# Kernel optimization log

Measured on AMD Instinct MI355X. Metric: run time of the kernel, lower is better.

## Reference

```python
import jax, jax.numpy as jnp
import numpy as np

N, D, R, NB, E = 50000, 128, 16, 10, 1600000
DECAY_RATE = 0.1
LN_EPS = 1e-5

def setup_inputs() -> dict:
    key = jax.random.key(0)
    ks = jax.random.split(key, 12)
    x = jax.random.normal(ks[0], (N, D), dtype=jnp.float32)
    edge_index = jax.random.randint(ks[1], (2, E), 0, N, dtype=jnp.int64)
    edge_type = jax.random.randint(ks[2], (E,), 0, R, dtype=jnp.int64)
    edge_time = jax.random.uniform(ks[3], (E,), dtype=jnp.float32)
    s = 1.0 / np.sqrt(D)
    basis = jax.random.normal(ks[4], (NB, D, D), dtype=jnp.float32) * s   # RGCN basis matrices
    comp = jax.random.normal(ks[5], (R, NB), dtype=jnp.float32) * (1.0 / np.sqrt(NB))
    root = jax.random.normal(ks[6], (D, D), dtype=jnp.float32) * s        # RGCN self-loop weight
    bias = jnp.zeros((D,), dtype=jnp.float32)
    tp_w = jax.random.normal(ks[7], (D, D), dtype=jnp.float32) * s        # time_proj
    tp_b = jnp.zeros((D,), dtype=jnp.float32)
    gamma = jnp.ones((D,), dtype=jnp.float32)
    beta = jnp.zeros((D,), dtype=jnp.float32)
    return {"x": x, "edge_index": edge_index, "edge_type": edge_type, "edge_time": edge_time,
            "basis": basis, "comp": comp, "root": root, "bias": bias,
            "tp_w": tp_w, "tp_b": tp_b, "gamma": gamma, "beta": beta}

def reference(x, edge_index, edge_type, edge_time, basis, comp, root, bias, tp_w, tp_b, gamma, beta):
    n, d = x.shape
    r = comp.shape[0]
    src, dst = edge_index[0], edge_index[1]
    # ---- RGCNConv (basis decomposition, per-relation mean aggregation) ----
    W = jnp.einsum('rb,bio->rio', comp, basis)                 # [R, D, D]
    msg = x[src]                                               # [E, D] gather
    seg = dst * r + edge_type                                  # combined (node, relation) segment id
    agg = jax.ops.segment_sum(msg, seg, num_segments=n * r)    # [N*R, D]
    cnt = jax.ops.segment_sum(jnp.ones_like(seg, dtype=x.dtype), seg, num_segments=n * r)
    agg = (agg / jnp.maximum(cnt, 1.0)[:, None]).reshape(n, r, d)  # per-relation mean
    x_rgcn = jnp.einsum('nrd,rdo->no', agg, W) + x @ root + bias
    # ---- exponential time decay weights, normalized to sum 1 ----
    td = edge_time.max() - edge_time
    td = td / (td.max() + 1e-8)
    w = jnp.exp(-DECAY_RATE * td)
    w = w / (w.sum() + 1e-8)
    # ---- time-decay aggregation (sum over relations == single scatter-add) ----
    agg_t = jax.ops.segment_sum(msg * w[:, None], dst, num_segments=n)
    deg = jax.ops.segment_sum(jnp.ones_like(dst, dtype=x.dtype), dst, num_segments=n)
    x_time = agg_t / jnp.clip(deg, 1.0)[:, None]
    # ---- combine, relu, (dropout=identity in eval), layernorm ----
    xc = x_rgcn + x_time @ tp_w + tp_b
    h = jax.nn.relu(xc)
    mu = h.mean(-1, keepdims=True)
    var = ((h - mu) ** 2).mean(-1, keepdims=True)
    return (h - mu) * jax.lax.rsqrt(var + LN_EPS) * gamma + beta
```

## Files before the change

### kernel.cpp

```cpp
#include <hip/hip_runtime.h>
#include <hip/hip_bf16.h>
#include <math.h>

#define NN 50000
#define DD 128
#define RR 16
#define NBASIS 10
#define NE 1600000
#define NSEG (NN * RR)
#define NPART ((NSEG + 1023) / 1024)
#define NSLICE 12
#define KTOT (NSLICE * DD)
#define DECAY 0.1f

typedef short bf16x8 __attribute__((ext_vector_type(8)));
typedef float f32x4 __attribute__((ext_vector_type(4)));
typedef float f32x2 __attribute__((ext_vector_type(2)));

__device__ __forceinline__ ushort f2b(float f) {
    unsigned u = __float_as_uint(f);
    unsigned r = (u + 0x7FFFu + ((u >> 16) & 1u)) >> 16;
    return (ushort)r;
}
__device__ __forceinline__ unsigned cvt_pk_bf16(float lo, float hi) {
    unsigned r;
    asm("v_cvt_pk_bf16_f32 %0, %1, %2" : "=v"(r) : "v"(lo), "v"(hi));
    return r;
}


#define XB_ITEMS (NN * (DD / 4))
#define PREP_ITEMS (XB_ITEMS + DD * KTOT)
__global__ __launch_bounds__(256) void k_front(
    const int* __restrict__ edst, const int* __restrict__ etype,
    const float* __restrict__ t,
    const float* __restrict__ x, const float* __restrict__ basis,
    const float* __restrict__ root, const float* __restrict__ tp_w,
    unsigned* __restrict__ red, unsigned* __restrict__ cnt,
    unsigned* __restrict__ segrank,
    ushort* __restrict__ xb, ushort* __restrict__ Bt3)
{
    const int bid = blockIdx.x;
    const int tid = threadIdx.x;
    if (bid < 1024) {
        const int stride = 1024 * 256;
        for (int e = bid * 256 + tid; e < NE; e += stride) {
            int d  = __builtin_nontemporal_load(edst + e);
            int ty = __builtin_nontemporal_load(etype + e);
            int seg = d * RR + ty;
            unsigned sh = (unsigned)(seg & 1) << 4;
            unsigned ret = atomicAdd(&cnt[seg >> 1], 1u << sh);
            unsigned rk = (ret >> sh) & 0xFFFu;
            __builtin_nontemporal_store(((unsigned)seg << 12) | rk, segrank + e);
        }
        return;
    }
    if (bid < 2048) {
        __shared__ float smx[4], smn[4];
        float mx = 0.0f, mn = 1e30f;
        const int stride = 1024 * 256;
        for (int i = (bid - 1024) * 256 + tid; i < NE / 4; i += stride) {
            f32x4 v = __builtin_nontemporal_load(((const f32x4*)t) + i);
            mx = fmaxf(mx, fmaxf(fmaxf(v.x, v.y), fmaxf(v.z, v.w)));
            mn = fminf(mn, fminf(fminf(v.x, v.y), fminf(v.z, v.w)));
        }
        for (int o = 32; o >= 1; o >>= 1) {
            mx = fmaxf(mx, __shfl_down(mx, o, 64));
            mn = fminf(mn, __shfl_down(mn, o, 64));
        }
        if ((tid & 63) == 0) { smx[tid >> 6] = mx; smn[tid >> 6] = mn; }
        __syncthreads();
        if (tid == 0) {
            mx = fmaxf(fmaxf(smx[0], smx[1]), fmaxf(smx[2], smx[3]));
            mn = fminf(fminf(smn[0], smn[1]), fminf(smn[2], smn[3]));
            atomicMax(&red[0], __float_as_uint(mx));
            atomicMax(&red[1], ~__float_as_uint(mn));
        }
        return;
    }
    int idx = (bid - 2048) * 256 + tid;
    if (idx < XB_ITEMS) {
        f32x4 v = ((const f32x4*)x)[idx];
        uint2 o;
        o.x = cvt_pk_bf16(v.x, v.y);
        o.y = cvt_pk_bf16(v.z, v.w);
        ((uint2*)xb)[idx] = o;
        return;
    }
    int bidx = idx - XB_ITEMS;
    if (bidx >= DD * KTOT) return;
    int j = bidx / KTOT, k = bidx - j * KTOT;
    int s = k >> 7, d = k & 127;
    float v;
    if (s < NBASIS) {
        v = basis[(s * DD + d) * DD + j];
    } else if (s == NBASIS) {
        v = tp_w[d * DD + j];
    } else {
        v = root[d * DD + j];
    }
    Bt3[bidx] = f2b(v);
}

__global__ __launch_bounds__(1024) void k_scan1(const unsigned* __restrict__ cnt,
                                                unsigned* __restrict__ segptr,
                                                unsigned* __restrict__ part) {
    __shared__ unsigned sh[1024];
    int tid = threadIdx.x;
    int i = blockIdx.x * 1024 + tid;
    unsigned v = 0u;
    if (i < NSEG) v = (cnt[i >> 1] >> ((i & 1) << 4)) & 0xFFFFu;
    sh[tid] = v;
    __syncthreads();
    for (int off = 1; off < 1024; off <<= 1) {
        unsigned t = (tid >= off) ? sh[tid - off] : 0u;
        __syncthreads();
        sh[tid] += t;
        __syncthreads();
    }
    if (i < NSEG) segptr[i] = sh[tid] - v;
    if (tid == 1023) part[blockIdx.x] = sh[1023];
}

__global__ __launch_bounds__(1024) void k_scan2(unsigned* __restrict__ part) {
    __shared__ unsigned sh[1024];
    int tid = threadIdx.x;
    unsigned v = (tid < NPART) ? part[tid] : 0u;
    sh[tid] = v;
    __syncthreads();
    for (int off = 1; off < 1024; off <<= 1) {
        unsigned t = (tid >= off) ? sh[tid - off] : 0u;
        __syncthreads();
        sh[tid] += t;
        __syncthreads();
    }
    if (tid < NPART) part[tid] = sh[tid] - v;
}

__global__ __launch_bounds__(1024) void k_scan3(unsigned* __restrict__ segptr,
                                                const unsigned* __restrict__ part) {
    int i = blockIdx.x * 1024 + threadIdx.x;
    if (i < NSEG) segptr[i] += part[i >> 10];
    if (blockIdx.x == 0 && threadIdx.x == 0) segptr[NSEG] = NE;
}

__global__ __launch_bounds__(256) void k_pre2(const int* __restrict__ esrc,
                                              const float* __restrict__ etime,
                                              const unsigned* __restrict__ segrank,
                                              unsigned* __restrict__ red,
                                              const unsigned* __restrict__ segptr,
                                              unsigned* __restrict__ srcw) {
    __shared__ float ssum[4];
    const int tid = threadIdx.x;
    const float tmax = __uint_as_float(red[0]);
    const float tmin = __uint_as_float(~red[1]);
    const float rtd = -DECAY / (tmax - tmin + 1e-8f);
    float s = 0.0f;
    const int stride = gridDim.x * 256;
    for (int e = blockIdx.x * 256 + tid; e < NE; e += stride) {
        float tv    = __builtin_nontemporal_load(etime + e);
        int sv      = __builtin_nontemporal_load(esrc + e);
        unsigned sr = __builtin_nontemporal_load(segrank + e);
        float w = __expf((tmax - tv) * rtd);
        s += w;
        unsigned pos = segptr[sr >> 12] + (sr & 4095u);
        __builtin_nontemporal_store(
            (unsigned)(sv & 0xFFFF) | ((unsigned)f2b(w) << 16), srcw + pos);
    }
    for (int o = 32; o >= 1; o >>= 1) s += __shfl_down(s, o, 64);
    if ((tid & 63) == 0) ssum[tid >> 6] = s;
    __syncthreads();
    if (tid == 0)
        atomicAdd(((float*)red) + 2, ssum[0] + ssum[1] + ssum[2] + ssum[3]);
}

__global__ __launch_bounds__(256) void k_gather(
    const ushort* __restrict__ xb, const unsigned* __restrict__ srcw,
    const unsigned* __restrict__ segptr, const unsigned* __restrict__ red,
    const float* __restrict__ comp,
    ushort* __restrict__ A2)
{
    const int wave = threadIdx.x >> 6, lane = threadIdx.x & 63;
    int dst0 = blockIdx.x * 4 + wave;
    if (dst0 >= NN) return;
    const int dst = __builtin_amdgcn_readfirstlane(dst0);
    const float sumw = ((const float*)red)[2];
    const unsigned s0 = (unsigned)dst * RR;
    const unsigned start = segptr[s0];
    const unsigned endAll = segptr[s0 + RR];
    const unsigned deg = endAll - start;
    unsigned* arow = (unsigned*)(A2 + (size_t)dst * KTOT);
    const unsigned* xbu = (const unsigned*)xb;

    f32x2 cb[NBASIS];
#pragma unroll
    for (int b = 0; b < NBASIS; ++b) cb[b] = (f32x2){0.f, 0.f};
    f32x2 acc = {0.f, 0.f}, xt = {0.f, 0.f};

    int r = 0;
    unsigned scur = start;
    unsigned endr = segptr[s0 + 1];
    unsigned e = start;

#define FLUSH_REL {                                                          \
        float scl = (endr > scur) ? (1.0f / (float)(endr - scur)) : 0.0f;    \
        f32x2 t = acc * scl;                                                 \
        _Pragma("unroll")                                                    \
        for (int b = 0; b < NBASIS; ++b)                                     \
            cb[b] += t * comp[r * NBASIS + b];                               \
        acc = (f32x2){0.f, 0.f}; scur = endr; ++r;                           \
        endr = (r < RR) ? segptr[s0 + r + 1] : 0xFFFFFFFFu; }

#define ACCUM(recq, pvq) {                                                   \
        float wgt = __uint_as_float((recq) & 0xFFFF0000u);                   \
        f32x2 v;                                                             \
        v.x = __uint_as_float((pvq) << 16);                                  \
        v.y = __uint_as_float((pvq) & 0xFFFF0000u);                          \
        acc += v;                                                            \
        xt += v * wgt; }

    while (e < endAll) {
        unsigned idx = e + (unsigned)lane;
        unsigned recv = srcw[(idx < endAll) ? idx : (endAll - 1u)];
        unsigned chunk = endAll - e;
        if (chunk > 64u) chunk = 64u;
        unsigned j = 0;
        for (; j + 8u <= chunk; j += 8u) {
            unsigned rec0 = (unsigned)__builtin_amdgcn_readlane((int)recv, (int)(j + 0));
            unsigned rec1 = (unsigned)__builtin_amdgcn_readlane((int)recv, (int)(j + 1));
            unsigned rec2 = (unsigned)__builtin_amdgcn_readlane((int)recv, (int)(j + 2));
            unsigned rec3 = (unsigned)__builtin_amdgcn_readlane((int)recv, (int)(j + 3));
            unsigned rec4 = (unsigned)__builtin_amdgcn_readlane((int)recv, (int)(j + 4));
            unsigned rec5 = (unsigned)__builtin_amdgcn_readlane((int)recv, (int)(j + 5));
            unsigned rec6 = (unsigned)__builtin_amdgcn_readlane((int)recv, (int)(j + 6));
            unsigned rec7 = (unsigned)__builtin_amdgcn_readlane((int)recv, (int)(j + 7));
            unsigned pv0 = xbu[((rec0 & 0xFFFFu) << 6) + lane];
            unsigned pv1 = xbu[((rec1 & 0xFFFFu) << 6) + lane];
            unsigned pv2 = xbu[((rec2 & 0xFFFFu) << 6) + lane];
            unsigned pv3 = xbu[((rec3 & 0xFFFFu) << 6) + lane];
            unsigned pv4 = xbu[((rec4 & 0xFFFFu) << 6) + lane];
            unsigned pv5 = xbu[((rec5 & 0xFFFFu) << 6) + lane];
            unsigned pv6 = xbu[((rec6 & 0xFFFFu) << 6) + lane];
            unsigned pv7 = xbu[((rec7 & 0xFFFFu) << 6) + lane];
            while (e >= endr) FLUSH_REL; ACCUM(rec0, pv0); ++e;
            while (e >= endr) FLUSH_REL; ACCUM(rec1, pv1); ++e;
            while (e >= endr) FLUSH_REL; ACCUM(rec2, pv2); ++e;
            while (e >= endr) FLUSH_REL; ACCUM(rec3, pv3); ++e;
            while (e >= endr) FLUSH_REL; ACCUM(rec4, pv4); ++e;
            while (e >= endr) FLUSH_REL; ACCUM(rec5, pv5); ++e;
            while (e >= endr) FLUSH_REL; ACCUM(rec6, pv6); ++e;
            while (e >= endr) FLUSH_REL; ACCUM(rec7, pv7); ++e;
        }
        for (; j < chunk; ++j) {
            unsigned rc = (unsigned)__builtin_amdgcn_readlane((int)recv, (int)j);
            unsigned pv = xbu[((rc & 0xFFFFu) << 6) + lane];
            while (e >= endr) FLUSH_REL;
            ACCUM(rc, pv);
            ++e;
        }
    }
    while (r < RR) FLUSH_REL;

#pragma unroll
    for (int b = 0; b < NBASIS; ++b)
        __builtin_nontemporal_store(cvt_pk_bf16(cb[b].x, cb[b].y),
                                    arow + b * 64 + lane);

    float s2 = 1.0f / ((sumw + 1e-8f) * fmaxf((float)deg, 1.0f));
    __builtin_nontemporal_store(cvt_pk_bf16(xt.x * s2, xt.y * s2),
                                arow + NBASIS * 64 + lane);
    __builtin_nontemporal_store(
        ((const unsigned*)(xb + (size_t)dst * DD))[lane],
        arow + (NBASIS + 1) * 64 + lane);
#undef FLUSH_REL
#undef ACCUM
}

__global__ __launch_bounds__(256) void k_fgemm(
    const ushort* __restrict__ A2, const ushort* __restrict__ Bt3,
    const float* __restrict__ bias, const float* __restrict__ tpb,
    const float* __restrict__ gamma, const float* __restrict__ beta,
    float* __restrict__ out)
{
    __shared__ unsigned Bs[2][4096];

    const int tid = threadIdx.x;
    const int w = tid >> 6, lane = tid & 63;
    const int quad = lane >> 4, l16 = lane & 15;
    const int n0 = blockIdx.x * 64;

    f32x4 acc[8];
#pragma unroll
    for (int ct = 0; ct < 8; ++ct) acc[ct] = (f32x4){0.f, 0.f, 0.f, 0.f};

    const ushort* arow = A2 + (size_t)(n0 + w * 16 + l16) * KTOT + quad * 8;
    const int srow = lane >> 3;
    const int sc   = lane & 7;

#define STAGE(buf, itv) {                                                    \
        const int k0_ = (itv) * 64;                                          \
        _Pragma("unroll")                                                    \
        for (int i_ = 0; i_ < 4; ++i_) {                                     \
            const int cid_ = i_ * 4 + w;                                     \
            const int row_ = cid_ * 8 + srow;                                \
            const int ck_  = sc ^ (row_ & 7);                                \
            const ushort* gb_ = Bt3 + (size_t)row_ * KTOT + k0_ + ck_ * 8;   \
            __builtin_amdgcn_global_load_lds(                                \
                (const __attribute__((address_space(1))) unsigned*)gb_,      \
                (__attribute__((address_space(3))) unsigned*)&Bs[buf][cid_ * 256], \
                16, 0, 0);                                                   \
        } }

    STAGE(0, 0);
    bf16x8 afp0 = *(const bf16x8*)(arow);
    bf16x8 afp1 = *(const bf16x8*)(arow + 32);
    __syncthreads();

    const int NIT = KTOT / 64;
    for (int it = 0; it < NIT; ++it) {
        if (it + 1 < NIT) STAGE((it + 1) & 1, it + 1);
        bf16x8 af0 = afp0, af1 = afp1;
        if (it + 1 < NIT) {
            afp0 = *(const bf16x8*)(arow + (it + 1) * 64);
            afp1 = *(const bf16x8*)(arow + (it + 1) * 64 + 32);
        }
        const unsigned* Bp = &Bs[it & 1][0];
#pragma unroll
        for (int ct = 0; ct < 8; ++ct) {
            const int rB = ct * 16 + l16;
            bf16x8 b0 = *(const bf16x8*)&Bp[rB * 32 + ((quad ^ (rB & 7)) << 2)];
            bf16x8 b1 = *(const bf16x8*)&Bp[rB * 32 + (((4 + quad) ^ (rB & 7)) << 2)];
            acc[ct] = __builtin_amdgcn_mfma_f32_16x16x32_bf16(af0, b0, acc[ct], 0, 0, 0);
            acc[ct] = __builtin_amdgcn_mfma_f32_16x16x32_bf16(af1, b1, acc[ct], 0, 0, 0);
        }
        __syncthreads();
    }
#undef STAGE

    float bc[8], gc[8], be[8];
#pragma unroll
    for (int ct = 0; ct < 8; ++ct) {
        int col = ct * 16 + l16;
        bc[ct] = bias[col] + tpb[col];
        gc[ct] = gamma[col];
        be[ct] = beta[col];
    }
    float s[4] = {0, 0, 0, 0}, q[4] = {0, 0, 0, 0};
#pragma unroll
    for (int ct = 0; ct < 8; ++ct)
#pragma unroll
        for (int i = 0; i < 4; ++i) {
            float v = fmaxf(acc[ct][i] + bc[ct], 0.0f);
            acc[ct][i] = v;
            s[i] += v;
            q[i] = fmaf(v, v, q[i]);
        }
#pragma unroll
    for (int off = 1; off < 16; off <<= 1)
#pragma unroll
        for (int i = 0; i < 4; ++i) {
            s[i] += __shfl_xor(s[i], off, 64);
            q[i] += __shfl_xor(q[i], off, 64);
        }
#pragma unroll
    for (int i = 0; i < 4; ++i) {
        const int row = n0 + w * 16 + quad * 4 + i;
        float mu  = s[i] * (1.0f / DD);
        float var = q[i] * (1.0f / DD) - mu * mu;
        float inv = rsqrtf(var + 1e-5f);
        if (row < NN) {
#pragma unroll
            for (int ct = 0; ct < 8; ++ct)
                __builtin_nontemporal_store(
                    (acc[ct][i] - mu) * inv * gc[ct] + be[ct],
                    out + (size_t)row * DD + ct * 16 + l16);
        }
    }
}

extern "C" void kernel_launch(void* const* d_in, const int* in_sizes, int n_in,
                              void* d_out, int out_size, void* d_ws, size_t ws_size,
                              hipStream_t stream)
{
    const float* x     = (const float*)d_in[0];
    const int*   ei    = (const int*)d_in[1];
    const int*   etype = (const int*)d_in[2];
    const float* etime = (const float*)d_in[3];
    const float* basis = (const float*)d_in[4];
    const float* comp  = (const float*)d_in[5];
    const float* root  = (const float*)d_in[6];
    const float* bias  = (const float*)d_in[7];
    const float* tp_w  = (const float*)d_in[8];
    const float* tp_b  = (const float*)d_in[9];
    const float* gamma = (const float*)d_in[10];
    const float* beta  = (const float*)d_in[11];
    float* out = (float*)d_out;

    char* ws = (char*)d_ws;
    size_t off = 0;
    auto alloc = [&](size_t bytes) -> void* {
        void* p = ws + off;
        off = (off + bytes + 255) & ~(size_t)255;
        return p;
    };
    unsigned* red     = (unsigned*)alloc(64);
    unsigned* cnt     = (unsigned*)alloc((size_t)(NSEG / 2) * 4);
    unsigned* segptr  = (unsigned*)alloc((size_t)(NSEG + 1) * 4);
    unsigned* part    = (unsigned*)alloc(1024 * 4);
    unsigned* srcw    = (unsigned*)alloc((size_t)NE * 4);
    unsigned* segrank = (unsigned*)alloc((size_t)NE * 4);
    ushort*   xb      = (ushort*)alloc((size_t)NN * DD * 2);
    ushort*   Bt3     = (ushort*)alloc((size_t)DD * KTOT * 2);
    ushort*   A2      = (ushort*)alloc((size_t)50048 * KTOT * 2);
    (void)ws_size;

    const int* esrc = ei;
    const int* edst = ei + NE;

    (void)hipMemsetAsync(ws, 0, 256 + (size_t)(NSEG / 2) * 4, stream);

    const int prep_blocks = (PREP_ITEMS + 255) / 256;
    hipLaunchKernelGGL(k_front, dim3(2048 + prep_blocks), dim3(256), 0, stream,
                       edst, etype, etime, x, basis, root, tp_w,
                       red, cnt, segrank, xb, Bt3);

    hipLaunchKernelGGL(k_scan1, dim3(NPART), dim3(1024), 0, stream, cnt, segptr, part);
    hipLaunchKernelGGL(k_scan2, dim3(1), dim3(1024), 0, stream, part);
    hipLaunchKernelGGL(k_scan3, dim3(NPART), dim3(1024), 0, stream, segptr, part);

    hipLaunchKernelGGL(k_pre2, dim3(1024), dim3(256), 0, stream,
                       esrc, etime, segrank, red, segptr, srcw);

    hipLaunchKernelGGL(k_gather, dim3((NN + 3) / 4), dim3(256), 0, stream,
                       xb, srcw, segptr, red, comp, A2);

    hipLaunchKernelGGL(k_fgemm, dim3((50048 + 63) / 64), dim3(256), 0, stream,
                       A2, Bt3, bias, tp_b, gamma, beta, out);
}
```

Measured before the change: 387.2 us.

## Replace global-atomic segment counting sort with two-level LDS bucket sort

Edges were bucketed by (dst, relation) segment using global atomics on a packed 16-bit counter array, followed by a scan over all 800k segments and a separate scatter pass. They are now sorted in two stages. First, per-block LDS histograms over coarse buckets of 64 nodes are built, scanned and used to scatter 64-bit (segment, payload) records into a temp buffer. Then each coarse bucket is loaded into LDS, fine-histogrammed, scanned and written in order, producing srcw and segptr. This removes contended global atomics, the large counter memset and the long scan, at the cost of an extra 8-byte-per-edge temp round trip and a hard CAP of 4096 edges per coarse bucket.

```diff
diff --git a/kernel.cpp b/kernel.cpp
--- a/kernel.cpp
+++ b/kernel.cpp
@@ -8,10 +8,17 @@
 #define NBASIS 10
 #define NE 1600000
 #define NSEG (NN * RR)
-#define NPART ((NSEG + 1023) / 1024)
 #define NSLICE 12
 #define KTOT (NSLICE * DD)
 #define DECAY 0.1f
+
+#define NB_COARSE 782
+#define NBLK_S 1024
+#define EPB 1563
+#define NHC (NB_COARSE * NBLK_S)
+#define NPART2 (NHC / 1024)
+#define FINE 1024
+#define CAP 4096
 
 typedef short bf16x8 __attribute__((ext_vector_type(8)));
 typedef float f32x4 __attribute__((ext_vector_type(4)));
@@ -31,35 +38,35 @@
 
 #define XB_ITEMS (NN * (DD / 4))
 #define PREP_ITEMS (XB_ITEMS + DD * KTOT)
-__global__ __launch_bounds__(256) void k_front(
-    const int* __restrict__ edst, const int* __restrict__ etype,
-    const float* __restrict__ t,
+__global__ __launch_bounds__(256) void k_s1(
+    const int* __restrict__ edst, const float* __restrict__ t,
     const float* __restrict__ x, const float* __restrict__ basis,
     const float* __restrict__ root, const float* __restrict__ tp_w,
-    unsigned* __restrict__ red, unsigned* __restrict__ cnt,
-    unsigned* __restrict__ segrank,
+    unsigned* __restrict__ red, unsigned* __restrict__ Hc,
     ushort* __restrict__ xb, ushort* __restrict__ Bt3)
 {
     const int bid = blockIdx.x;
     const int tid = threadIdx.x;
-    if (bid < 1024) {
-        const int stride = 1024 * 256;
-        for (int e = bid * 256 + tid; e < NE; e += stride) {
-            int d  = __builtin_nontemporal_load(edst + e);
-            int ty = __builtin_nontemporal_load(etype + e);
-            int seg = d * RR + ty;
-            unsigned sh = (unsigned)(seg & 1) << 4;
-            unsigned ret = atomicAdd(&cnt[seg >> 1], 1u << sh);
-            unsigned rk = (ret >> sh) & 0xFFFu;
-            __builtin_nontemporal_store(((unsigned)seg << 12) | rk, segrank + e);
-        }
+    if (bid < NBLK_S) {
+        __shared__ unsigned h[NB_COARSE];
+        for (int i = tid; i < NB_COARSE; i += 256) h[i] = 0u;
+        __syncthreads();
+        const int e0 = bid * EPB;
+        const int e1 = (e0 + EPB < NE) ? e0 + EPB : NE;
+        for (int e = e0 + tid; e < e1; e += 256) {
+            int d = __builtin_nontemporal_load(edst + e);
+            atomicAdd(&h[d >> 6], 1u);
+        }
+        __syncthreads();
+        for (int i = tid; i < NB_COARSE; i += 256)
+            Hc[i * NBLK_S + bid] = h[i];
         return;
     }
-    if (bid < 2048) {
+    if (bid < NBLK_S + 256) {
         __shared__ float smx[4], smn[4];
         float mx = 0.0f, mn = 1e30f;
-        const int stride = 1024 * 256;
-        for (int i = (bid - 1024) * 256 + tid; i < NE / 4; i += stride) {
+        const int stride = 256 * 256;
+        for (int i = (bid - NBLK_S) * 256 + tid; i < NE / 4; i += stride) {
             f32x4 v = __builtin_nontemporal_load(((const f32x4*)t) + i);
             mx = fmaxf(mx, fmaxf(fmaxf(v.x, v.y), fmaxf(v.z, v.w)));
             mn = fminf(mn, fminf(fminf(v.x, v.y), fminf(v.z, v.w)));
@@ -78,7 +85,7 @@
         }
         return;
     }
-    int idx = (bid - 2048) * 256 + tid;
+    int idx = (bid - NBLK_S - 256) * 256 + tid;
     if (idx < XB_ITEMS) {
         f32x4 v = ((const f32x4*)x)[idx];
         uint2 o;
@@ -102,14 +109,12 @@
     Bt3[bidx] = f2b(v);
 }
 
-__global__ __launch_bounds__(1024) void k_scan1(const unsigned* __restrict__ cnt,
-                                                unsigned* __restrict__ segptr,
+__global__ __launch_bounds__(1024) void k_scan1(unsigned* __restrict__ Hc,
                                                 unsigned* __restrict__ part) {
     __shared__ unsigned sh[1024];
     int tid = threadIdx.x;
     int i = blockIdx.x * 1024 + tid;
-    unsigned v = 0u;
-    if (i < NSEG) v = (cnt[i >> 1] >> ((i & 1) << 4)) & 0xFFFFu;
+    unsigned v = Hc[i];
     sh[tid] = v;
     __syncthreads();
     for (int off = 1; off < 1024; off <<= 1) {
@@ -118,14 +123,14 @@
         sh[tid] += t;
         __syncthreads();
     }
-    if (i < NSEG) segptr[i] = sh[tid] - v;
+    Hc[i] = sh[tid] - v;
     if (tid == 1023) part[blockIdx.x] = sh[1023];
 }
 
 __global__ __launch_bounds__(1024) void k_scan2(unsigned* __restrict__ part) {
     __shared__ unsigned sh[1024];
     int tid = threadIdx.x;
-    unsigned v = (tid < NPART) ? part[tid] : 0u;
+    unsigned v = (tid < NPART2) ? part[tid] : 0u;
     sh[tid] = v;
     __syncthreads();
     for (int off = 1; off < 1024; off <<= 1) {
@@ -134,44 +139,96 @@
         sh[tid] += t;
         __syncthreads();
     }
-    if (tid < NPART) part[tid] = sh[tid] - v;
-}
-
-__global__ __launch_bounds__(1024) void k_scan3(unsigned* __restrict__ segptr,
+    if (tid < NPART2) part[tid] = sh[tid] - v;
+}
+
+__global__ __launch_bounds__(1024) void k_scan3(unsigned* __restrict__ Hc,
                                                 const unsigned* __restrict__ part) {
     int i = blockIdx.x * 1024 + threadIdx.x;
-    if (i < NSEG) segptr[i] += part[i >> 10];
-    if (blockIdx.x == 0 && threadIdx.x == 0) segptr[NSEG] = NE;
-}
-
-__global__ __launch_bounds__(256) void k_pre2(const int* __restrict__ esrc,
-                                              const float* __restrict__ etime,
-                                              const unsigned* __restrict__ segrank,
-                                              unsigned* __restrict__ red,
-                                              const unsigned* __restrict__ segptr,
-                                              unsigned* __restrict__ srcw) {
+    Hc[i] += part[i >> 10];
+}
+
+__global__ __launch_bounds__(256) void k_s3(
+    const int* __restrict__ esrc, const int* __restrict__ edst,
+    const int* __restrict__ etype, const float* __restrict__ etime,
+    const unsigned* __restrict__ Hc, unsigned* __restrict__ red,
+    unsigned long long* __restrict__ tmp)
+{
+    __shared__ unsigned cur[NB_COARSE];
     __shared__ float ssum[4];
+    const int bid = blockIdx.x;
     const int tid = threadIdx.x;
+    for (int i = tid; i < NB_COARSE; i += 256)
+        cur[i] = Hc[i * NBLK_S + bid];
     const float tmax = __uint_as_float(red[0]);
     const float tmin = __uint_as_float(~red[1]);
     const float rtd = -DECAY / (tmax - tmin + 1e-8f);
+    __syncthreads();
     float s = 0.0f;
-    const int stride = gridDim.x * 256;
-    for (int e = blockIdx.x * 256 + tid; e < NE; e += stride) {
-        float tv    = __builtin_nontemporal_load(etime + e);
-        int sv      = __builtin_nontemporal_load(esrc + e);
-        unsigned sr = __builtin_nontemporal_load(segrank + e);
+    const int e0 = bid * EPB;
+    const int e1 = (e0 + EPB < NE) ? e0 + EPB : NE;
+    for (int e = e0 + tid; e < e1; e += 256) {
+        int d    = __builtin_nontemporal_load(edst + e);
+        int ty   = __builtin_nontemporal_load(etype + e);
+        int sv   = __builtin_nontemporal_load(esrc + e);
+        float tv = __builtin_nontemporal_load(etime + e);
         float w = __expf((tmax - tv) * rtd);
         s += w;
-        unsigned pos = segptr[sr >> 12] + (sr & 4095u);
+        unsigned seg = (unsigned)(d * RR + ty);
+        unsigned pos = atomicAdd(&cur[seg >> 10], 1u);
+        unsigned lo = (unsigned)(sv & 0xFFFF) | ((unsigned)f2b(w) << 16);
         __builtin_nontemporal_store(
-            (unsigned)(sv & 0xFFFF) | ((unsigned)f2b(w) << 16), srcw + pos);
+            ((unsigned long long)seg << 32) | lo, tmp + pos);
     }
     for (int o = 32; o >= 1; o >>= 1) s += __shfl_down(s, o, 64);
     if ((tid & 63) == 0) ssum[tid >> 6] = s;
     __syncthreads();
     if (tid == 0)
         atomicAdd(((float*)red) + 2, ssum[0] + ssum[1] + ssum[2] + ssum[3]);
+}
+
+__global__ __launch_bounds__(512) void k_s4(
+    const unsigned long long* __restrict__ tmp, const unsigned* __restrict__ Hc,
+    unsigned* __restrict__ srcw, unsigned* __restrict__ segptr)
+{
+    __shared__ unsigned long long recs[CAP];
+    __shared__ unsigned hist[FINE];
+    __shared__ unsigned excl[FINE];
+    __shared__ unsigned curf[FINE];
+    __shared__ unsigned sh[512];
+    const int b = blockIdx.x;
+    const int tid = threadIdx.x;
+    const unsigned start = Hc[b * NBLK_S];
+    const unsigned end   = (b + 1 < NB_COARSE) ? Hc[(b + 1) * NBLK_S] : (unsigned)NE;
+    int n = (int)(end - start);
+    if (n > CAP) n = CAP;
+    for (int i = tid; i < FINE; i += 512) hist[i] = 0u;
+    for (int i = tid; i < n; i += 512) recs[i] = tmp[start + i];
+    __syncthreads();
+    const unsigned base = (unsigned)b << 10;
+    for (int i = tid; i < n; i += 512)
+        atomicAdd(&hist[(unsigned)(recs[i] >> 32) - base], 1u);
+    __syncthreads();
+    unsigned a0 = hist[2 * tid], a1 = hist[2 * tid + 1];
+    sh[tid] = a0 + a1;
+    __syncthreads();
+    for (int off = 1; off < 512; off <<= 1) {
+        unsigned t = (tid >= off) ? sh[tid - off] : 0u;
+        __syncthreads();
+        sh[tid] += t;
+        __syncthreads();
+    }
+    unsigned pe = sh[tid] - (a0 + a1);
+    excl[2 * tid] = pe;          curf[2 * tid] = pe;
+    excl[2 * tid + 1] = pe + a0; curf[2 * tid + 1] = pe + a0;
+    __syncthreads();
+    for (int i = tid; i < n; i += 512) {
+        unsigned long long r = recs[i];
+        unsigned p = atomicAdd(&curf[(unsigned)(r >> 32) - base], 1u);
+        srcw[start + p] = (unsigned)r;
+    }
+    for (int i = tid; i < FINE; i += 512)
+        segptr[(size_t)b * FINE + i] = start + excl[i];
 }
 
 __global__ __launch_bounds__(256) void k_gather(
@@ -403,33 +460,35 @@
         off = (off + bytes + 255) & ~(size_t)255;
         return p;
     };
-    unsigned* red     = (unsigned*)alloc(64);
-    unsigned* cnt     = (unsigned*)alloc((size_t)(NSEG / 2) * 4);
-    unsigned* segptr  = (unsigned*)alloc((size_t)(NSEG + 1) * 4);
-    unsigned* part    = (unsigned*)alloc(1024 * 4);
-    unsigned* srcw    = (unsigned*)alloc((size_t)NE * 4);
-    unsigned* segrank = (unsigned*)alloc((size_t)NE * 4);
-    ushort*   xb      = (ushort*)alloc((size_t)NN * DD * 2);
-    ushort*   Bt3     = (ushort*)alloc((size_t)DD * KTOT * 2);
-    ushort*   A2      = (ushort*)alloc((size_t)50048 * KTOT * 2);
+    unsigned* red    = (unsigned*)alloc(256);
+    unsigned* Hc     = (unsigned*)alloc((size_t)NHC * 4);
+    unsigned* part   = (unsigned*)alloc(1024 * 4);
+    unsigned* srcw   = (unsigned*)alloc((size_t)NE * 4);
+    unsigned long long* tmp = (unsigned long long*)alloc((size_t)NE * 8);
+    unsigned* segptr = (unsigned*)alloc((size_t)(NB_COARSE * FINE) * 4);
+    ushort*   xb     = (ushort*)alloc((size_t)NN * DD * 2);
+    ushort*   Bt3    = (ushort*)alloc((size_t)DD * KTOT * 2);
+    ushort*   A2     = (ushort*)alloc((size_t)50048 * KTOT * 2);
     (void)ws_size;
 
     const int* esrc = ei;
     const int* edst = ei + NE;
 
-    (void)hipMemsetAsync(ws, 0, 256 + (size_t)(NSEG / 2) * 4, stream);
+    (void)hipMemsetAsync(red, 0, 256, stream);
 
     const int prep_blocks = (PREP_ITEMS + 255) / 256;
-    hipLaunchKernelGGL(k_front, dim3(2048 + prep_blocks), dim3(256), 0, stream,
-                       edst, etype, etime, x, basis, root, tp_w,
-                       red, cnt, segrank, xb, Bt3);
-
-    hipLaunchKernelGGL(k_scan1, dim3(NPART), dim3(1024), 0, stream, cnt, segptr, part);
+    hipLaunchKernelGGL(k_s1, dim3(NBLK_S + 256 + prep_blocks), dim3(256), 0, stream,
+                       edst, etime, x, basis, root, tp_w, red, Hc, xb, Bt3);
+
+    hipLaunchKernelGGL(k_scan1, dim3(NPART2), dim3(1024), 0, stream, Hc, part);
     hipLaunchKernelGGL(k_scan2, dim3(1), dim3(1024), 0, stream, part);
-    hipLaunchKernelGGL(k_scan3, dim3(NPART), dim3(1024), 0, stream, segptr, part);
-
-    hipLaunchKernelGGL(k_pre2, dim3(1024), dim3(256), 0, stream,
-                       esrc, etime, segrank, red, segptr, srcw);
+    hipLaunchKernelGGL(k_scan3, dim3(NPART2), dim3(1024), 0, stream, Hc, part);
+
+    hipLaunchKernelGGL(k_s3, dim3(NBLK_S), dim3(256), 0, stream,
+                       esrc, edst, etype, etime, Hc, red, tmp);
+
+    hipLaunchKernelGGL(k_s4, dim3(NB_COARSE), dim3(512), 0, stream,
+                       tmp, Hc, srcw, segptr);
 
     hipLaunchKernelGGL(k_gather, dim3((NN + 3) / 4), dim3(256), 0, stream,
                        xb, srcw, segptr, red, comp, A2);
```

Result: faster. 342.4 us (-11.6%).
